# Performance work log

Measured on AMD Instinct MI355X. Metric: run time of the kernel, lower is better.

Reference implementation:

```python
import jax, jax.numpy as jnp
import numpy as np

NUM_SENTENCES = 32
MAX_SENT_LEN = 64
EMBED_DIM = 768
BATCH = 16
TEXT_LEN = NUM_SENTENCES * MAX_SENT_LEN  # 2048


def setup_inputs() -> dict:
    key = jax.random.key(0)
    k1, k2 = jax.random.split(key)
    inputs = jax.random.normal(k1, (BATCH, TEXT_LEN, EMBED_DIM), dtype=jnp.float32)
    W = jax.random.normal(k2, (EMBED_DIM, 2 * NUM_SENTENCES), dtype=jnp.float32) * 0.02
    b = jnp.zeros((2 * NUM_SENTENCES,), dtype=jnp.float32)
    return {"inputs": inputs, "W": W, "b": b}


def reference(inputs, W, b):
    B, T, E = inputs.shape
    S, L = NUM_SENTENCES, MAX_SENT_LEN

    # offsets from mean-pooled input through Dense(2*S)
    pooled = jnp.mean(inputs, axis=1)                      # [B, E]
    offsets = pooled @ W + b                               # [B, 2S]
    # clip to [0, L-1], cast (truncation == floor for nonneg values)
    start_off = jnp.clip(offsets[:, :S], 0.0, float(L - 1)).astype(jnp.int32)  # [B, S]
    end_off = jnp.clip(offsets[:, S:], 0.0, float(L - 1)).astype(jnp.int32)    # [B, S]

    base = (jnp.arange(S, dtype=jnp.int32) * L)[None, :]   # [1, S]
    start_idx = jnp.clip(base + start_off, 0, T - L)        # [B, S]
    end_idx = jnp.clip(base + L + end_off, start_idx, T)    # [B, S]

    # vectorized slice+pad: position j of sentence i comes from start_idx+j,
    # valid while j < (end_idx - start_idx) and j < L (pad/truncate to L)
    j = jnp.arange(L, dtype=jnp.int32)                      # [L]
    gather_idx = start_idx[:, :, None] + j[None, None, :]   # [B, S, L]
    valid = j[None, None, :] < (end_idx - start_idx)[:, :, None]  # [B, S, L]

    flat_idx = jnp.clip(gather_idx, 0, T - 1).reshape(B, S * L)
    gathered = jnp.take_along_axis(inputs, flat_idx[:, :, None], axis=1)
    gathered = gathered.reshape(B, S, L, E)
    out = jnp.where(valid[:, :, :, None], gathered, jnp.zeros((), inputs.dtype))
    return out
```

## Files before the change

kernel.cpp:

```cpp
#include <hip/hip_runtime.h>

#define BATCH 16
#define T_LEN 2048
#define E_DIM 768
#define E4 (E_DIM / 4)
#define N_SENT 32
#define S_LEN 64
#define NCHUNK 64
#define RPC (T_LEN / NCHUNK)

typedef float v4f __attribute__((ext_vector_type(4)));

__global__ void pool_partial(const v4f* __restrict__ in4, v4f* __restrict__ partial4) {
    const int tx = threadIdx.x;
    const int b  = blockIdx.x;
    const int tc = blockIdx.y;
    const v4f* p = in4 + ((size_t)b * T_LEN + (size_t)tc * RPC) * E4 + tx;
    v4f s = (v4f){0.f, 0.f, 0.f, 0.f};
#pragma unroll 8
    for (int t = 0; t < RPC; ++t) s += p[(size_t)t * E4];
    partial4[((size_t)tc * BATCH + b) * E4 + tx] = s;
}

__global__ void compute_idx(const v4f* __restrict__ partial4,
                            const float* __restrict__ W,
                            const float* __restrict__ bias,
                            int* __restrict__ sidx, int* __restrict__ eidx) {
    __shared__ float pooled[E_DIM];
    __shared__ float colsum[4][2 * N_SENT];
    __shared__ int   offi[2 * N_SENT];
    const int b   = blockIdx.x;
    const int tid = threadIdx.x;

    if (tid < E4) {
        v4f s = (v4f){0.f, 0.f, 0.f, 0.f};
#pragma unroll 8
        for (int tc = 0; tc < NCHUNK; ++tc)
            s += partial4[((size_t)tc * BATCH + b) * E4 + tid];
        const float inv = 1.0f / (float)T_LEN;
        ((v4f*)pooled)[tid] = s * inv;
    }
    __syncthreads();

    const int c = tid & 63;
    const int q = tid >> 6;
    float acc = 0.f;
    const float* pb = pooled + q * 192;
    const float* Wq = W + (size_t)q * 192 * (2 * N_SENT) + c;
#pragma unroll 8
    for (int e = 0; e < 192; ++e) acc += pb[e] * Wq[(size_t)e * (2 * N_SENT)];
    colsum[q][c] = acc;
    __syncthreads();

    if (tid < 2 * N_SENT) {
        float o = bias[tid] + colsum[0][tid] + colsum[1][tid] + colsum[2][tid] + colsum[3][tid];
        float cl = fminf(fmaxf(o, 0.f), (float)(S_LEN - 1));
        offi[tid] = (int)cl;
    }
    __syncthreads();

    if (tid < N_SENT) {
        const int so   = offi[tid];
        const int eo   = offi[N_SENT + tid];
        const int base = tid * S_LEN;
        int si = min(base + so, T_LEN - S_LEN);
        int ei = min(max(base + S_LEN + eo, si), T_LEN);
        sidx[b * N_SENT + tid] = si;
        eidx[b * N_SENT + tid] = ei;
    }
}

__global__ void gather_rows(const v4f* __restrict__ in4,
                            const int* __restrict__ sidx,
                            const int* __restrict__ eidx,
                            v4f* __restrict__ out4) {
    const int wave = threadIdx.x >> 6;
    const int lane = threadIdx.x & 63;
    const int row0 = blockIdx.x * 32 + wave * 8;
#pragma unroll
    for (int r = 0; r < 8; ++r) {
        const int row = row0 + r;
        const int j = row & (S_LEN - 1);
        const int s = (row >> 6) & (N_SENT - 1);
        const int b = row >> 11;
        const int si = sidx[b * N_SENT + s];
        const int ei = eidx[b * N_SENT + s];
        const bool valid = j < (ei - si);
        const v4f* src = in4 + ((size_t)b * T_LEN + (si + j)) * E4 + lane;
        v4f* dst = out4 + (size_t)row * E4 + lane;
#pragma unroll
        for (int seg = 0; seg < 3; ++seg) {
            v4f v = (v4f){0.f, 0.f, 0.f, 0.f};
            if (valid) v = src[seg * 64];
            __builtin_nontemporal_store(v, dst + seg * 64);
        }
    }
}

extern "C" void kernel_launch(void* const* d_in, const int* in_sizes, int n_in,
                              void* d_out, int out_size, void* d_ws, size_t ws_size,
                              hipStream_t stream) {
    const v4f*   in4  = (const v4f*)d_in[0];
    const float* W    = (const float*)d_in[1];
    const float* bias = (const float*)d_in[2];
    v4f* out4 = (v4f*)d_out;

    v4f* partial4 = (v4f*)d_ws;
    int* sidx = (int*)((char*)d_ws + (size_t)NCHUNK * BATCH * E4 * sizeof(v4f));
    int* eidx = sidx + BATCH * N_SENT;

    pool_partial<<<dim3(BATCH, NCHUNK), 192, 0, stream>>>(in4, partial4);
    compute_idx<<<BATCH, 256, 0, stream>>>(partial4, W, bias, sidx, eidx);
    gather_rows<<<dim3(BATCH * N_SENT * S_LEN / 32), 256, 0, stream>>>(
        in4, sidx, eidx, out4);
}
```

Baseline: 208.5 us.

## Fuse pooling, index computation and gather into one cooperative kernel with grid sync

```diff
diff --git a/kernel.cpp b/kernel.cpp
--- a/kernel.cpp
+++ b/kernel.cpp
@@ -1,4 +1,7 @@
 #include <hip/hip_runtime.h>
+#include <hip/hip_cooperative_groups.h>
+
+namespace cg = cooperative_groups;
 
 #define BATCH 16
 #define T_LEN 2048
@@ -11,88 +14,95 @@
 
 typedef float v4f __attribute__((ext_vector_type(4)));
 
-__global__ void pool_partial(const v4f* __restrict__ in4, v4f* __restrict__ partial4) {
-    const int tx = threadIdx.x;
-    const int b  = blockIdx.x;
-    const int tc = blockIdx.y;
-    const v4f* p = in4 + ((size_t)b * T_LEN + (size_t)tc * RPC) * E4 + tx;
-    v4f s = (v4f){0.f, 0.f, 0.f, 0.f};
-#pragma unroll 8
-    for (int t = 0; t < RPC; ++t) s += p[(size_t)t * E4];
-    partial4[((size_t)tc * BATCH + b) * E4 + tx] = s;
-}
-
-__global__ void compute_idx(const v4f* __restrict__ partial4,
-                            const float* __restrict__ W,
-                            const float* __restrict__ bias,
-                            int* __restrict__ sidx, int* __restrict__ eidx) {
-    __shared__ float pooled[E_DIM];
-    __shared__ float colsum[4][2 * N_SENT];
-    __shared__ int   offi[2 * N_SENT];
-    const int b   = blockIdx.x;
+__global__ void __launch_bounds__(256, 4)
+fused(const v4f* __restrict__ in4,
+      const float* __restrict__ W,
+      const float* __restrict__ bias,
+      v4f* __restrict__ partial4,
+      int* __restrict__ sidx, int* __restrict__ eidx,
+      v4f* __restrict__ out4) {
+    cg::grid_group grid = cg::this_grid();
     const int tid = threadIdx.x;
 
-    if (tid < E4) {
-        v4f s = (v4f){0.f, 0.f, 0.f, 0.f};
+    {
+        const int b  = blockIdx.x >> 6;
+        const int tc = blockIdx.x & (NCHUNK - 1);
+        if (tid < E4) {
+            const v4f* p = in4 + ((size_t)b * T_LEN + (size_t)tc * RPC) * E4 + tid;
+            v4f s = (v4f){0.f, 0.f, 0.f, 0.f};
 #pragma unroll 8
-        for (int tc = 0; tc < NCHUNK; ++tc)
-            s += partial4[((size_t)tc * BATCH + b) * E4 + tid];
-        const float inv = 1.0f / (float)T_LEN;
-        ((v4f*)pooled)[tid] = s * inv;
+            for (int t = 0; t < RPC; ++t) s += p[(size_t)t * E4];
+            partial4[((size_t)tc * BATCH + b) * E4 + tid] = s;
+        }
     }
-    __syncthreads();
+    grid.sync();
 
-    const int c = tid & 63;
-    const int q = tid >> 6;
-    float acc = 0.f;
-    const float* pb = pooled + q * 192;
-    const float* Wq = W + (size_t)q * 192 * (2 * N_SENT) + c;
+    if (blockIdx.x < BATCH) {
+        __shared__ float pooled[E_DIM];
+        __shared__ float colsum[4][2 * N_SENT];
+        __shared__ int   offi[2 * N_SENT];
+        const int b = blockIdx.x;
+
+        if (tid < E4) {
+            v4f s = (v4f){0.f, 0.f, 0.f, 0.f};
 #pragma unroll 8
-    for (int e = 0; e < 192; ++e) acc += pb[e] * Wq[(size_t)e * (2 * N_SENT)];
-    colsum[q][c] = acc;
-    __syncthreads();
+            for (int tc = 0; tc < NCHUNK; ++tc)
+                s += partial4[((size_t)tc * BATCH + b) * E4 + tid];
+            const float inv = 1.0f / (float)T_LEN;
+            ((v4f*)pooled)[tid] = s * inv;
+        }
+        __syncthreads();
 
-    if (tid < 2 * N_SENT) {
-        float o = bias[tid] + colsum[0][tid] + colsum[1][tid] + colsum[2][tid] + colsum[3][tid];
-        float cl = fminf(fmaxf(o, 0.f), (float)(S_LEN - 1));
-        offi[tid] = (int)cl;
+        const int c = tid & 63;
+        const int q = tid >> 6;
+        float acc = 0.f;
+        const float* pb = pooled + q * 192;
+        const float* Wq = W + (size_t)q * 192 * (2 * N_SENT) + c;
+#pragma unroll 8
+        for (int e = 0; e < 192; ++e) acc += pb[e] * Wq[(size_t)e * (2 * N_SENT)];
+        colsum[q][c] = acc;
+        __syncthreads();
+
+        if (tid < 2 * N_SENT) {
+            float o = bias[tid] + colsum[0][tid] + colsum[1][tid] + colsum[2][tid] + colsum[3][tid];
+            float cl = fminf(fmaxf(o, 0.f), (float)(S_LEN - 1));
+            offi[tid] = (int)cl;
+        }
+        __syncthreads();
+
+        if (tid < N_SENT) {
+            const int so   = offi[tid];
+            const int eo   = offi[N_SENT + tid];
+            const int base = tid * S_LEN;
+            int si = min(base + so, T_LEN - S_LEN);
+            int ei = min(max(base + S_LEN + eo, si), T_LEN);
+            sidx[b * N_SENT + tid] = si;
+            eidx[b * N_SENT + tid] = ei;
+        }
     }
-    __syncthreads();
+    grid.sync();
 
-    if (tid < N_SENT) {
-        const int so   = offi[tid];
-        const int eo   = offi[N_SENT + tid];
-        const int base = tid * S_LEN;
-        int si = min(base + so, T_LEN - S_LEN);
-        int ei = min(max(base + S_LEN + eo, si), T_LEN);
-        sidx[b * N_SENT + tid] = si;
-        eidx[b * N_SENT + tid] = ei;
-    }
-}
-
-__global__ void gather_rows(const v4f* __restrict__ in4,
-                            const int* __restrict__ sidx,
-                            const int* __restrict__ eidx,
-                            v4f* __restrict__ out4) {
-    const int wave = threadIdx.x >> 6;
-    const int lane = threadIdx.x & 63;
-    const int row0 = blockIdx.x * 32 + wave * 8;
+    {
+        const int wave = tid >> 6;
+        const int lane = tid & 63;
+        const int row0 = blockIdx.x * 32 + wave * 8;
 #pragma unroll
-    for (int r = 0; r < 8; ++r) {
-        const int row = row0 + r;
-        const int j = row & (S_LEN - 1);
-        const int s = (row >> 6) & (N_SENT - 1);
-        const int b = row >> 11;
-        const int si = sidx[b * N_SENT + s];
-        const int ei = eidx[b * N_SENT + s];
-        const bool valid = j < (ei - si);
-        const v4f* src = in4 + ((size_t)b * T_LEN + (si + j)) * E4 + lane;
-        v4f* dst = out4 + (size_t)row * E4 + lane;
+        for (int r = 0; r < 8; ++r) {
+            const int row = row0 + r;
+            const int j = row & (S_LEN - 1);
+            const int s = (row >> 6) & (N_SENT - 1);
+            const int b = row >> 11;
+            const int si = sidx[b * N_SENT + s];
+            const int ei = eidx[b * N_SENT + s];
+            const bool valid = j < (ei - si);
+            const v4f* src = in4 + ((size_t)b * T_LEN + (si + j)) * E4 + lane;
+            v4f* dst = out4 + (size_t)row * E4 + lane;
 #pragma unroll
-        for (int seg = 0; seg < 3; ++seg) {
-            v4f v = (v4f){0.f, 0.f, 0.f, 0.f};
-            if (valid) v = src[seg * 64];
-            __builtin_nontemporal_store(v, dst + seg * 64);
+            for (int seg = 0; seg < 3; ++seg) {
+                v4f v = (v4f){0.f, 0.f, 0.f, 0.f};
+                if (valid) v = src[seg * 64];
+                dst[seg * 64] = v;
+            }
         }
     }
 }
@@ -109,8 +119,8 @@
     int* sidx = (int*)((char*)d_ws + (size_t)NCHUNK * BATCH * E4 * sizeof(v4f));
     int* eidx = sidx + BATCH * N_SENT;
 
-    pool_partial<<<dim3(BATCH, NCHUNK), 192, 0, stream>>>(in4, partial4);
-    compute_idx<<<BATCH, 256, 0, stream>>>(partial4, W, bias, sidx, eidx);
-    gather_rows<<<dim3(BATCH * N_SENT * S_LEN / 32), 256, 0, stream>>>(
-        in4, sidx, eidx, out4);
+    void* args[] = {(void*)&in4, (void*)&W, (void*)&bias,
+                    (void*)&partial4, (void*)&sidx, (void*)&eidx, (void*)&out4};
+    hipLaunchCooperativeKernel((const void*)fused, dim3(BATCH * NCHUNK), dim3(256),
+                               args, 0, stream);
 }
```

After: 422.6 us. 103% more time.
